# Optimization experiments

Hardware: AMD Instinct MI355X
Metric: run time of the kernel (lower is better)

Reference implementation:

```python
import jax, jax.numpy as jnp
import numpy as np

EPS = 1e-5
NEG = -1e9

def rmsnorm(x, g, eps=EPS):
    x32 = x.astype(jnp.float32)
    n = x32 * jax.lax.rsqrt(jnp.mean(x32 * x32, axis=-1, keepdims=True) + eps)
    return g * n.astype(x.dtype)

def setup_inputs() -> dict:
    key = jax.random.key(0)
    ks = jax.random.split(key, 10)
    B, S, D, H = 2, 2048, 768, 12
    F = 4 * D
    s = 0.02
    return {
        "x": jax.random.normal(ks[0], (B, S, D), jnp.float32),
        "mask": jax.random.randint(ks[1], (B, S, S), 0, 2, jnp.int32),
        "wq": jax.random.normal(ks[2], (D, D), jnp.float32) * s,
        "wk": jax.random.normal(ks[3], (D, D), jnp.float32) * s,
        "wv": jax.random.normal(ks[4], (D, D), jnp.float32) * s,
        "wo": jax.random.normal(ks[5], (D, D), jnp.float32) * s,
        "w1": jax.random.normal(ks[6], (F, D), jnp.float32) * s,
        "w2": jax.random.normal(ks[7], (D, F), jnp.float32) * s,
        "w3": jax.random.normal(ks[8], (F, D), jnp.float32) * s,
        "g_attn": jnp.ones((D,), jnp.float32),
        "g_ffn": jnp.ones((D,), jnp.float32),
    }

def reference(x, mask, wq, wk, wv, wo, w1, w2, w3, g_attn, g_ffn):
    B, S, D = x.shape
    H = 12
    Dk = D // H
    # --- attention sub-block (pre-norm) ---
    xn = rmsnorm(x, g_attn)
    # torch Linear: y = x @ W^T; split heads -> [B,H,S,Dk]
    q = (xn @ wq.T).reshape(B, S, H, Dk).transpose(0, 2, 1, 3)
    k = (xn @ wk.T).reshape(B, S, H, Dk).transpose(0, 2, 1, 3)
    v = (xn @ wv.T).reshape(B, S, H, Dk).transpose(0, 2, 1, 3)
    scores = jnp.einsum("bhqd,bhkd->bhqk", q, k) / jnp.sqrt(jnp.float32(Dk))
    scores = jnp.where(mask[:, None, :, :] == 0, jnp.float32(NEG), scores)
    probs = jax.nn.softmax(scores, axis=-1)  # dropout p=0.0 -> identity
    attn = jnp.einsum("bhqk,bhkd->bhqd", probs, v)
    attn = attn.transpose(0, 2, 1, 3).reshape(B, S, D)
    h = x + attn @ wo.T
    # --- SwiGLU FFN sub-block (pre-norm) ---
    hn = rmsnorm(h, g_ffn)
    ffn = (jax.nn.silu(hn @ w1.T) * (hn @ w3.T)) @ w2.T
    return h + ffn
```

## Files before the change

### kernel.cpp

```cpp
#include <hip/hip_runtime.h>
#include <hip/hip_bf16.h>

#define S_LEN 2048
#define D_MODEL 768
#define NH 12
#define DK 64
#define F_DIM 3072
#define BATCH 2
#define M_ROWS (BATCH * S_LEN)

typedef __bf16 bf16x8 __attribute__((ext_vector_type(8)));
typedef float floatx4 __attribute__((ext_vector_type(4)));
typedef unsigned short u16;
typedef unsigned long long u64;

__device__ inline float bf2f(u16 u) {
    union { unsigned int i; float f; } x; x.i = ((unsigned int)u) << 16; return x.f;
}
__device__ inline u16 f2bf(float f) {
    union { float f; unsigned int i; } x; x.f = f;
    unsigned int r = x.i + 0x7fffu + ((x.i >> 16) & 1u);
    return (u16)(r >> 16);
}
__device__ __forceinline__ bf16x8 as_bf16x8(uint4 v) {
    union { uint4 u; bf16x8 b; } c; c.u = v; return c.b;
}

__device__ __forceinline__ void ldsload16(const u16* g, u16* l) {
    __builtin_amdgcn_global_load_lds(
        (const __attribute__((address_space(1))) unsigned int*)g,
        (__attribute__((address_space(3))) unsigned int*)l, 16, 0, 0);
}

__global__ __launch_bounds__(256)
void cvt_all(const float4* __restrict__ wq, const float4* __restrict__ wk,
             const float4* __restrict__ wv, const float4* __restrict__ wo,
             const float4* __restrict__ w1, const float4* __restrict__ w2,
             const float4* __restrict__ w3,
             ushort4* wqb, ushort4* wkb, ushort4* wvb, ushort4* wob,
             ushort4* w13f, ushort4* w2b) {
    const int WS4 = (D_MODEL * D_MODEL) / 4;
    const int WB4 = (F_DIM * D_MODEL) / 4;
    const int RW4 = D_MODEL / 4;
    int i = blockIdx.x * 256 + threadIdx.x;
    const float4* src; ushort4* dst; int off, doff;
    if (i < 4 * WS4) {
        int s = i / WS4; off = i - s * WS4; doff = off;
        src = (s == 0) ? wq : (s == 1) ? wk : (s == 2) ? wv : wo;
        dst = (s == 0) ? wqb : (s == 1) ? wkb : (s == 2) ? wvb : wob;
    } else {
        int j = i - 4 * WS4; int s = j / WB4; off = j - s * WB4;
        if (s == 1) { src = w2; dst = w2b; doff = off; }
        else {
            src = (s == 0) ? w1 : w3;
            dst = w13f;
            int which = (s == 0) ? 0 : 1;
            int row = off / RW4, c4 = off - row * RW4;
            int k = c4 * 4;
            int n_tile = row >> 4, nl = row & 15;
            int k_tile = k >> 5, quad = (k >> 3) & 3, jj = k & 7;
            int lane = quad * 16 + nl;
            int f = (n_tile * 24 + k_tile) * 2 + which;
            doff = (f * 512 + lane * 8 + jj) >> 2;
        }
    }
    float4 v = src[off];
    ushort4 o;
    o.x = f2bf(v.x); o.y = f2bf(v.y); o.z = f2bf(v.z); o.w = f2bf(v.w);
    dst[doff] = o;
}

__global__ __launch_bounds__(256)
void mask_bits(const int* __restrict__ m, u64* __restrict__ bits) {
    size_t gid = (size_t)blockIdx.x * 256 + threadIdx.x;
    u64 b = __ballot(m[gid] != 0);
    if ((threadIdx.x & 63) == 0) bits[gid >> 6] = b;
}

__global__ __launch_bounds__(256)
void rmsnorm_k(const float* __restrict__ x, const float* __restrict__ g, u16* __restrict__ out) {
    int row = blockIdx.x;
    const float* xr = x + (size_t)row * D_MODEL;
    u16* orow = out + (size_t)row * D_MODEL;
    int t = threadIdx.x;
    float v0 = xr[t];
    float v1 = xr[t + 256];
    float v2 = xr[t + 512];
    float ss = v0 * v0 + v1 * v1 + v2 * v2;
    #pragma unroll
    for (int off = 1; off < 64; off <<= 1) ss += __shfl_xor(ss, off);
    __shared__ float red[4];
    if ((t & 63) == 0) red[t >> 6] = ss;
    __syncthreads();
    float tot = red[0] + red[1] + red[2] + red[3];
    float scale = rsqrtf(tot * (1.0f / (float)D_MODEL) + 1e-5f);
    orow[t]       = f2bf(g[t]       * v0 * scale);
    orow[t + 256] = f2bf(g[t + 256] * v1 * scale);
    orow[t + 512] = f2bf(g[t + 512] * v2 * scale);
}

__global__ __launch_bounds__(256, 3)
void gemm_f1(const u16* __restrict__ A, const u16* __restrict__ W13f,
             u16* __restrict__ Cout) {
    const int K = D_MODEL, N = F_DIM;
    __shared__ u16 As[2][64][32];

    int t = threadIdx.x;
    int w = t >> 6, lane = t & 63;
    int lrow = lane & 15, quad = lane >> 4;

    int lid = blockIdx.y * 24 + blockIdx.x;
    int xcd = lid & 7, s = lid >> 3;
    int nb = xcd * 3 + (s % 3);
    int mb = s / 3;
    int mBase = mb * 64;
    int ntile0 = nb * 8 + w * 2;

    int srow = lane >> 2, scol = (lane & 3) * 8;
    const u16* Ag = A + (size_t)(mBase + w * 16 + srow) * K + scol;
    const uint4* Bf = (const uint4*)W13f;

    auto stageA = [&](int k0, int b) {
        ldsload16(Ag + k0, &As[b][w * 16][0]);
    };

    floatx4 zero = {0.f, 0.f, 0.f, 0.f};
    floatx4 acc[4][2], acc2[4][2];
    #pragma unroll
    for (int r = 0; r < 4; ++r)
        #pragma unroll
        for (int c = 0; c < 2; ++c) { acc[r][c] = zero; acc2[r][c] = zero; }

    stageA(0, 0);
    int cur = 0;
    for (int kt = 0; kt < 24; ++kt) {
        uint4 b1v[2], b3v[2];
        #pragma unroll
        for (int c = 0; c < 2; ++c) {
            int f = ((ntile0 + c) * 24 + kt) * 2;
            b1v[c] = Bf[(size_t)f * 64 + lane];
            b3v[c] = Bf[(size_t)(f + 1) * 64 + lane];
        }
        __syncthreads();
        if (kt + 1 < 24) stageA((kt + 1) * 32, cur ^ 1);

        bf16x8 af[4];
        #pragma unroll
        for (int r = 0; r < 4; ++r) af[r] = *(const bf16x8*)&As[cur][r * 16 + lrow][quad * 8];
        #pragma unroll
        for (int c = 0; c < 2; ++c) {
            bf16x8 b1f = as_bf16x8(b1v[c]);
            bf16x8 b3f = as_bf16x8(b3v[c]);
            #pragma unroll
            for (int r = 0; r < 4; ++r) {
                acc[r][c]  = __builtin_amdgcn_mfma_f32_16x16x32_bf16(af[r], b1f, acc[r][c], 0, 0, 0);
                acc2[r][c] = __builtin_amdgcn_mfma_f32_16x16x32_bf16(af[r], b3f, acc2[r][c], 0, 0, 0);
            }
        }
        cur ^= 1;
    }

    #pragma unroll
    for (int r = 0; r < 4; ++r) {
        #pragma unroll
        for (int c = 0; c < 2; ++c) {
            #pragma unroll
            for (int j = 0; j < 4; ++j) {
                int grow = mBase + r * 16 + quad * 4 + j;
                int gcol = nb * 128 + w * 32 + c * 16 + lrow;
                float a = acc[r][c][j];
                Cout[(size_t)grow * N + gcol] = f2bf((a / (1.0f + __expf(-a))) * acc2[r][c][j]);
            }
        }
    }
}

__global__ __launch_bounds__(256, 3)
void gemm64(const u16* __restrict__ A, const u16* __restrict__ B1,
            const float* __restrict__ R, float* __restrict__ Cout, int N, int K) {
    __shared__ u16 As[2][64][32];
    __shared__ u16 Bs[2][64][32];

    int t = threadIdx.x;
    int w = t >> 6, lane = t & 63;
    int mBase = blockIdx.y * 64, nBase = blockIdx.x * 64;
    int lrow = lane & 15, quad = lane >> 4;
    int wm = (w >> 1) * 32, wn = (w & 1) * 32;

    int srow = lane >> 2, scol = (lane & 3) * 8;
    const u16* Ag = A  + (size_t)(mBase + w * 16 + srow) * K + scol;
    const u16* Bg = B1 + (size_t)(nBase + w * 16 + srow) * K + scol;

    auto stage = [&](int k0, int b) {
        ldsload16(Ag + k0, &As[b][w * 16][0]);
        ldsload16(Bg + k0, &Bs[b][w * 16][0]);
    };

    floatx4 zero = {0.f, 0.f, 0.f, 0.f};
    floatx4 acc[2][2];
    #pragma unroll
    for (int r = 0; r < 2; ++r)
        #pragma unroll
        for (int c = 0; c < 2; ++c) acc[r][c] = zero;

    stage(0, 0);
    int cur = 0;
    for (int k0 = 0; k0 < K; k0 += 32) {
        __syncthreads();
        if (k0 + 32 < K) stage(k0 + 32, cur ^ 1);

        bf16x8 af[2], bf[2];
        #pragma unroll
        for (int r = 0; r < 2; ++r) af[r] = *(const bf16x8*)&As[cur][wm + r * 16 + lrow][quad * 8];
        #pragma unroll
        for (int c = 0; c < 2; ++c) bf[c] = *(const bf16x8*)&Bs[cur][wn + c * 16 + lrow][quad * 8];
        #pragma unroll
        for (int r = 0; r < 2; ++r)
            #pragma unroll
            for (int c = 0; c < 2; ++c)
                acc[r][c] = __builtin_amdgcn_mfma_f32_16x16x32_bf16(af[r], bf[c], acc[r][c], 0, 0, 0);
        cur ^= 1;
    }

    #pragma unroll
    for (int r = 0; r < 2; ++r) {
        #pragma unroll
        for (int c = 0; c < 2; ++c) {
            #pragma unroll
            for (int j = 0; j < 4; ++j) {
                int grow = mBase + wm + r * 16 + quad * 4 + j;
                int gcol = nBase + wn + c * 16 + lrow;
                size_t idx = (size_t)grow * N + gcol;
                Cout[idx] = acc[r][c][j] + R[idx];
            }
        }
    }
}

__global__ __launch_bounds__(256, 4)
void gemm_qkv(const u16* __restrict__ A, const u16* __restrict__ wq,
              const u16* __restrict__ wk, const u16* __restrict__ wv,
              u16* __restrict__ qb, u16* __restrict__ kb, u16* __restrict__ vt) {
    const int K = D_MODEL;
    __shared__ u16 As[2][64][32];
    __shared__ u16 Bs[2][128][32];

    int t = threadIdx.x;
    int w = t >> 6, lane = t & 63;
    int nb = blockIdx.x;
    int which = nb / 6;
    int mBase = blockIdx.y * 64, nBase = (nb % 6) * 128;
    const u16* B1 = (which == 0) ? wq : (which == 1) ? wk : wv;
    int lrow = lane & 15, quad = lane >> 4;
    int wm = (w >> 1) * 32, wn = (w & 1) * 64;

    int srow = lane >> 2, scol = (lane & 3) * 8;
    const u16* Ag = A  + (size_t)(mBase + w * 16 + srow) * K + scol;
    const u16* Bg = B1 + (size_t)(nBase + w * 32 + srow) * K + scol;

    auto stage = [&](int k0, int b) {
        ldsload16(Ag + k0, &As[b][w * 16][0]);
        ldsload16(Bg + k0, &Bs[b][w * 32][0]);
        ldsload16(Bg + (size_t)16 * K + k0, &Bs[b][w * 32 + 16][0]);
    };

    floatx4 zero = {0.f, 0.f, 0.f, 0.f};
    floatx4 acc[2][4];
    #pragma unroll
    for (int r = 0; r < 2; ++r)
        #pragma unroll
        for (int c = 0; c < 4; ++c) acc[r][c] = zero;

    stage(0, 0);
    int cur = 0;
    for (int k0 = 0; k0 < K; k0 += 32) {
        __syncthreads();
        if (k0 + 32 < K) stage(k0 + 32, cur ^ 1);
        bf16x8 af[2];
        #pragma unroll
        for (int r = 0; r < 2; ++r) af[r] = *(const bf16x8*)&As[cur][wm + r * 16 + lrow][quad * 8];
        #pragma unroll
        for (int c = 0; c < 4; ++c) {
            bf16x8 bfr = *(const bf16x8*)&Bs[cur][wn + c * 16 + lrow][quad * 8];
            #pragma unroll
            for (int r = 0; r < 2; ++r)
                acc[r][c] = __builtin_amdgcn_mfma_f32_16x16x32_bf16(af[r], bfr, acc[r][c], 0, 0, 0);
        }
        cur ^= 1;
    }

    u16* dst = (which == 0) ? qb : kb;
    const float qscale = 0.18033688011112042f;
    #pragma unroll
    for (int r = 0; r < 2; ++r) {
        #pragma unroll
        for (int c = 0; c < 4; ++c) {
            #pragma unroll
            for (int j = 0; j < 4; ++j) {
                int grow = mBase + wm + r * 16 + quad * 4 + j;
                int gcol = nBase + wn + c * 16 + lrow;
                float val = acc[r][c][j];
                if (which == 2) {
                    int bb = grow >> 11, s = grow & 2047;
                    int hh = gcol >> 6, d = gcol & 63;
                    vt[((((size_t)bb * NH + hh) * DK + d) << 11) + s] = f2bf(val);
                } else {
                    if (which == 0) val *= qscale;
                    dst[(size_t)grow * D_MODEL + gcol] = f2bf(val);
                }
            }
        }
    }
}

__global__ __launch_bounds__(256)
void attn_mfma(const u16* __restrict__ q, const u16* __restrict__ k,
               const u16* __restrict__ vt, const u64* __restrict__ mbits,
               u16* __restrict__ out) {
    __shared__ u16 Qs0[64][32], Qs1[64][32];
    __shared__ u16 Ks0[64][32], Ks1[64][32];
    __shared__ u16 Vs0[64][32], Vs1[64][32];
    __shared__ u16 PT[4][16][72];

    int t = threadIdx.x;
    int lane = t & 63;
    int w = t >> 6;
    int lrow = lane & 15;
    int quad = lane >> 4;

    int st0 = blockIdx.x * 64;
    int bh = blockIdx.y;
    int h = bh % NH;
    int b = bh / NH;

    const u16* qbase = q + ((size_t)b * S_LEN + st0) * D_MODEL + h * DK;
    const u16* kbase = k + (size_t)b * S_LEN * D_MODEL + h * DK;
    const u16* vbase = vt + (size_t)bh * DK * S_LEN;
    const u64* bw = mbits + ((size_t)b * S_LEN + st0 + w * 16 + lrow) * (S_LEN / 64);

    int srow = lane >> 2;
    int scol = (lane & 3) * 8;

    const u16* qg = qbase + (size_t)(w * 16 + srow) * D_MODEL + scol;
    ldsload16(qg, &Qs0[w * 16][0]);
    ldsload16(qg + 32, &Qs1[w * 16][0]);
    __syncthreads();
    bf16x8 bq0 = *(const bf16x8*)&Qs0[w * 16 + lrow][quad * 8];
    bf16x8 bq1 = *(const bf16x8*)&Qs1[w * 16 + lrow][quad * 8];

    const u16* kg = kbase + (size_t)(w * 16 + srow) * D_MODEL + scol;
    const u16* vg = vbase + (size_t)(w * 16 + srow) * S_LEN + scol;

    bf16x8 ones;
    {
        union { u16 u; __bf16 b; } o; o.u = 0x3F80;
        #pragma unroll
        for (int j = 0; j < 8; ++j) ones[j] = o.b;
    }

    floatx4 zero = {0.f, 0.f, 0.f, 0.f};
    floatx4 Ot[4] = {zero, zero, zero, zero};
    floatx4 Osum = zero;

    for (int kt = 0; kt < S_LEN; kt += 64) {
        u64 mw = bw[kt >> 6];
        unsigned mlo = (unsigned)mw, mhi = (unsigned)(mw >> 32);
        __syncthreads();
        ldsload16(kg + (size_t)kt * D_MODEL, &Ks0[w * 16][0]);
        ldsload16(kg + (size_t)kt * D_MODEL + 32, &Ks1[w * 16][0]);
        ldsload16(vg + kt, &Vs0[w * 16][0]);
        ldsload16(vg + kt + 32, &Vs1[w * 16][0]);
        __syncthreads();

        floatx4 st[4];
        #pragma unroll
        for (int nt = 0; nt < 4; ++nt) {
            bf16x8 ak0 = *(const bf16x8*)&Ks0[nt * 16 + lrow][quad * 8];
            bf16x8 ak1 = *(const bf16x8*)&Ks1[nt * 16 + lrow][quad * 8];
            st[nt] = __builtin_amdgcn_mfma_f32_16x16x32_bf16(ak0, bq0, zero, 0, 0, 0);
            st[nt] = __builtin_amdgcn_mfma_f32_16x16x32_bf16(ak1, bq1, st[nt], 0, 0, 0);
        }

        #pragma unroll
        for (int nt = 0; nt < 4; ++nt) {
            unsigned half = (nt & 2) ? mhi : mlo;
            unsigned tmp = half >> ((nt & 1) * 16 + quad * 4);
            unsigned eu[4];
            #pragma unroll
            for (int j = 0; j < 4; ++j) {
                float e = __builtin_amdgcn_exp2f(st[nt][j]);
                unsigned msk = (unsigned)((int)(tmp << (31 - j)) >> 31);
                eu[j] = __float_as_uint(e) & msk;
            }
            uint2 p;
            p.x = (eu[0] >> 16) | (eu[1] & 0xffff0000u);
            p.y = (eu[2] >> 16) | (eu[3] & 0xffff0000u);
            *(uint2*)&PT[w][lrow][nt * 16 + quad * 4] = p;
        }

        bf16x8 ap0 = *(const bf16x8*)&PT[w][lrow][quad * 8];
        bf16x8 ap1 = *(const bf16x8*)&PT[w][lrow][32 + quad * 8];
        Osum = __builtin_amdgcn_mfma_f32_16x16x32_bf16(ap0, ones, Osum, 0, 0, 0);
        Osum = __builtin_amdgcn_mfma_f32_16x16x32_bf16(ap1, ones, Osum, 0, 0, 0);
        #pragma unroll
        for (int dt = 0; dt < 4; ++dt) {
            bf16x8 bv0 = *(const bf16x8*)&Vs0[dt * 16 + lrow][quad * 8];
            bf16x8 bv1 = *(const bf16x8*)&Vs1[dt * 16 + lrow][quad * 8];
            Ot[dt] = __builtin_amdgcn_mfma_f32_16x16x32_bf16(ap0, bv0, Ot[dt], 0, 0, 0);
            Ot[dt] = __builtin_amdgcn_mfma_f32_16x16x32_bf16(ap1, bv1, Ot[dt], 0, 0, 0);
        }
    }

    float invj[4];
    #pragma unroll
    for (int j = 0; j < 4; ++j) invj[j] = 1.0f / Osum[j];

    u16* obase = out + ((size_t)b * S_LEN + st0 + w * 16) * D_MODEL + h * DK;
    #pragma unroll
    for (int dt = 0; dt < 4; ++dt)
        #pragma unroll
        for (int j = 0; j < 4; ++j)
            obase[(size_t)(quad * 4 + j) * D_MODEL + dt * 16 + lrow] = f2bf(Ot[dt][j] * invj[j]);
}

extern "C" void kernel_launch(void* const* d_in, const int* in_sizes, int n_in,
                              void* d_out, int out_size, void* d_ws, size_t ws_size,
                              hipStream_t stream) {
    const float* x      = (const float*)d_in[0];
    const int*   mask   = (const int*)d_in[1];
    const float* wq     = (const float*)d_in[2];
    const float* wk     = (const float*)d_in[3];
    const float* wv     = (const float*)d_in[4];
    const float* wo     = (const float*)d_in[5];
    const float* w1     = (const float*)d_in[6];
    const float* w2     = (const float*)d_in[7];
    const float* w3     = (const float*)d_in[8];
    const float* g_attn = (const float*)d_in[9];
    const float* g_ffn  = (const float*)d_in[10];
    float* out = (float*)d_out;

    const size_t WSMALL = (size_t)D_MODEL * D_MODEL;
    const size_t WBIG   = (size_t)F_DIM * D_MODEL;
    const size_t MD     = (size_t)M_ROWS * D_MODEL;

    char* ws = (char*)d_ws;
    u16* wqb  = (u16*)ws;            ws += WSMALL * 2;
    u16* wkb  = (u16*)ws;            ws += WSMALL * 2;
    u16* wvb  = (u16*)ws;            ws += WSMALL * 2;
    u16* wob  = (u16*)ws;            ws += WSMALL * 2;
    u16* w13f = (u16*)ws;            ws += WBIG * 2 * 2;
    u16* w2b  = (u16*)ws;            ws += WBIG * 2;
    u16* xn  = (u16*)ws;             ws += MD * 2;
    u16* qb  = (u16*)ws;             ws += MD * 2;
    u16* kb  = (u16*)ws;             ws += MD * 2;
    u16* vb  = (u16*)ws;             ws += MD * 2;
    u16* ao  = (u16*)ws;             ws += MD * 2;
    float* hb = (float*)ws;          ws += MD * 4;
    u64* mb  = (u64*)ws;             ws += (size_t)BATCH * S_LEN * (S_LEN / 64) * 8;
    u16* hn = xn;
    u16* ub = qb;
    (void)ws_size; (void)n_in; (void)in_sizes; (void)out_size;

    dim3 blk(256);

    cvt_all<<<9216, blk, 0, stream>>>((const float4*)wq, (const float4*)wk, (const float4*)wv,
                                      (const float4*)wo, (const float4*)w1, (const float4*)w2,
                                      (const float4*)w3,
                                      (ushort4*)wqb, (ushort4*)wkb, (ushort4*)wvb, (ushort4*)wob,
                                      (ushort4*)w13f, (ushort4*)w2b);
    mask_bits<<<(BATCH * S_LEN * S_LEN) / 256, blk, 0, stream>>>(mask, mb);

    rmsnorm_k<<<M_ROWS, blk, 0, stream>>>(x, g_attn, xn);
    gemm_qkv<<<dim3(18, M_ROWS / 64), blk, 0, stream>>>(xn, wqb, wkb, wvb, qb, kb, vb);
    attn_mfma<<<dim3(S_LEN / 64, BATCH * NH), blk, 0, stream>>>(qb, kb, vb, mb, ao);
    gemm64<<<dim3(D_MODEL / 64, M_ROWS / 64), blk, 0, stream>>>(ao, wob, x, hb, D_MODEL, D_MODEL);
    rmsnorm_k<<<M_ROWS, blk, 0, stream>>>((const float*)hb, g_ffn, hn);
    gemm_f1<<<dim3(24, M_ROWS / 64), blk, 0, stream>>>(hn, w13f, ub);
    gemm64<<<dim3(D_MODEL / 64, M_ROWS / 64), blk, 0, stream>>>(ub, w2b, hb, out, D_MODEL, F_DIM);
}
```

Measured before the change: 360.1 us.

## Pre-swizzle all weights into MFMA fragment layout and load B directly from global

Result: no change. 366.0 us (+1.6%).

```diff
diff --git a/kernel.cpp b/kernel.cpp
--- a/kernel.cpp
+++ b/kernel.cpp
@@ -37,31 +37,35 @@
              const float4* __restrict__ wv, const float4* __restrict__ wo,
              const float4* __restrict__ w1, const float4* __restrict__ w2,
              const float4* __restrict__ w3,
-             ushort4* wqb, ushort4* wkb, ushort4* wvb, ushort4* wob,
-             ushort4* w13f, ushort4* w2b) {
+             ushort4* wqf, ushort4* wkf, ushort4* wvf, ushort4* wof,
+             ushort4* w13f, ushort4* w2f) {
     const int WS4 = (D_MODEL * D_MODEL) / 4;
     const int WB4 = (F_DIM * D_MODEL) / 4;
-    const int RW4 = D_MODEL / 4;
     int i = blockIdx.x * 256 + threadIdx.x;
     const float4* src; ushort4* dst; int off, doff;
     if (i < 4 * WS4) {
-        int s = i / WS4; off = i - s * WS4; doff = off;
+        int s = i / WS4; off = i - s * WS4;
         src = (s == 0) ? wq : (s == 1) ? wk : (s == 2) ? wv : wo;
-        dst = (s == 0) ? wqb : (s == 1) ? wkb : (s == 2) ? wvb : wob;
+        dst = (s == 0) ? wqf : (s == 1) ? wkf : (s == 2) ? wvf : wof;
+        int row = off / 192, c4 = off - row * 192;
+        int k = c4 * 4;
+        int lane = ((k >> 3) & 3) * 16 + (row & 15);
+        doff = (((row >> 4) * 24 + (k >> 5)) * 512 + lane * 8 + (k & 7)) >> 2;
     } else {
         int j = i - 4 * WS4; int s = j / WB4; off = j - s * WB4;
-        if (s == 1) { src = w2; dst = w2b; doff = off; }
-        else {
-            src = (s == 0) ? w1 : w3;
-            dst = w13f;
+        if (s == 1) {
+            src = w2; dst = w2f;
+            int row = off / 768, c4 = off - row * 768;
+            int k = c4 * 4;
+            int lane = ((k >> 3) & 3) * 16 + (row & 15);
+            doff = (((row >> 4) * 96 + (k >> 5)) * 512 + lane * 8 + (k & 7)) >> 2;
+        } else {
             int which = (s == 0) ? 0 : 1;
-            int row = off / RW4, c4 = off - row * RW4;
+            src = (s == 0) ? w1 : w3; dst = w13f;
+            int row = off / 192, c4 = off - row * 192;
             int k = c4 * 4;
-            int n_tile = row >> 4, nl = row & 15;
-            int k_tile = k >> 5, quad = (k >> 3) & 3, jj = k & 7;
-            int lane = quad * 16 + nl;
-            int f = (n_tile * 24 + k_tile) * 2 + which;
-            doff = (f * 512 + lane * 8 + jj) >> 2;
+            int lane = ((k >> 3) & 3) * 16 + (row & 15);
+            doff = ((((row >> 4) * 24 + (k >> 5)) * 2 + which) * 512 + lane * 8 + (k & 7)) >> 2;
         }
     }
     float4 v = src[off];
@@ -103,7 +107,7 @@
 void gemm_f1(const u16* __restrict__ A, const u16* __restrict__ W13f,
              u16* __restrict__ Cout) {
     const int K = D_MODEL, N = F_DIM;
-    __shared__ u16 As[2][64][32];
+    __shared__ u16 As[2][4][512];
 
     int t = threadIdx.x;
     int w = t >> 6, lane = t & 63;
@@ -112,17 +116,12 @@
     int lid = blockIdx.y * 24 + blockIdx.x;
     int xcd = lid & 7, s = lid >> 3;
     int nb = xcd * 3 + (s % 3);
-    int mb = s / 3;
-    int mBase = mb * 64;
+    int mBase = (s / 3) * 64;
     int ntile0 = nb * 8 + w * 2;
 
-    int srow = lane >> 2, scol = (lane & 3) * 8;
-    const u16* Ag = A + (size_t)(mBase + w * 16 + srow) * K + scol;
+    const u16* Ag = A + (size_t)(mBase + w * 16 + lrow) * K + quad * 8;
     const uint4* Bf = (const uint4*)W13f;
-
-    auto stageA = [&](int k0, int b) {
-        ldsload16(Ag + k0, &As[b][w * 16][0]);
-    };
+    auto stageA = [&](int k0, int b) { ldsload16(Ag + k0, &As[b][w][0]); };
 
     floatx4 zero = {0.f, 0.f, 0.f, 0.f};
     floatx4 acc[4][2], acc2[4][2];
@@ -146,7 +145,7 @@
 
         bf16x8 af[4];
         #pragma unroll
-        for (int r = 0; r < 4; ++r) af[r] = *(const bf16x8*)&As[cur][r * 16 + lrow][quad * 8];
+        for (int r = 0; r < 4; ++r) af[r] = *(const bf16x8*)&As[cur][r][lane * 8];
         #pragma unroll
         for (int c = 0; c < 2; ++c) {
             bf16x8 b1f = as_bf16x8(b1v[c]);
@@ -175,26 +174,22 @@
     }
 }
 
-__global__ __launch_bounds__(256, 3)
-void gemm64(const u16* __restrict__ A, const u16* __restrict__ B1,
-            const float* __restrict__ R, float* __restrict__ Cout, int N, int K) {
-    __shared__ u16 As[2][64][32];
-    __shared__ u16 Bs[2][64][32];
+__global__ __launch_bounds__(256, 4)
+void gemm_nf(const u16* __restrict__ A, const u16* __restrict__ Bw,
+             const float* __restrict__ R, float* __restrict__ Cout, int N, int K) {
+    const int KT = K >> 5;
+    __shared__ u16 As[2][4][512];
 
     int t = threadIdx.x;
     int w = t >> 6, lane = t & 63;
+    int lrow = lane & 15, quad = lane >> 4;
     int mBase = blockIdx.y * 64, nBase = blockIdx.x * 64;
-    int lrow = lane & 15, quad = lane >> 4;
-    int wm = (w >> 1) * 32, wn = (w & 1) * 32;
-
-    int srow = lane >> 2, scol = (lane & 3) * 8;
-    const u16* Ag = A  + (size_t)(mBase + w * 16 + srow) * K + scol;
-    const u16* Bg = B1 + (size_t)(nBase + w * 16 + srow) * K + scol;
-
-    auto stage = [&](int k0, int b) {
-        ldsload16(Ag + k0, &As[b][w * 16][0]);
-        ldsload16(Bg + k0, &Bs[b][w * 16][0]);
-    };
+    int wm = (w >> 1) * 2, wn = (w & 1) * 2;
+    int ntile0 = (nBase >> 4) + wn;
+
+    const u16* Ag = A + (size_t)(mBase + w * 16 + lrow) * K + quad * 8;
+    const uint4* Bf = (const uint4*)Bw;
+    auto stageA = [&](int k0, int b) { ldsload16(Ag + k0, &As[b][w][0]); };
 
     floatx4 zero = {0.f, 0.f, 0.f, 0.f};
     floatx4 acc[2][2];
@@ -203,22 +198,26 @@
         #pragma unroll
         for (int c = 0; c < 2; ++c) acc[r][c] = zero;
 
-    stage(0, 0);
+    stageA(0, 0);
     int cur = 0;
-    for (int k0 = 0; k0 < K; k0 += 32) {
+    for (int kt = 0; kt < KT; ++kt) {
+        uint4 bv[2];
+        #pragma unroll
+        for (int c = 0; c < 2; ++c)
+            bv[c] = Bf[(size_t)((ntile0 + c) * KT + kt) * 64 + lane];
         __syncthreads();
-        if (k0 + 32 < K) stage(k0 + 32, cur ^ 1);
-
-        bf16x8 af[2], bf[2];
-        #pragma unroll
-        for (int r = 0; r < 2; ++r) af[r] = *(const bf16x8*)&As[cur][wm + r * 16 + lrow][quad * 8];
-        #pragma unroll
-        for (int c = 0; c < 2; ++c) bf[c] = *(const bf16x8*)&Bs[cur][wn + c * 16 + lrow][quad * 8];
-        #pragma unroll
-        for (int r = 0; r < 2; ++r)
-            #pragma unroll
-            for (int c = 0; c < 2; ++c)
-                acc[r][c] = __builtin_amdgcn_mfma_f32_16x16x32_bf16(af[r], bf[c], acc[r][c], 0, 0, 0);
+        if (kt + 1 < KT) stageA((kt + 1) * 32, cur ^ 1);
+
+        bf16x8 af[2];
+        #pragma unroll
+        for (int r = 0; r < 2; ++r) af[r] = *(const bf16x8*)&As[cur][wm + r][lane * 8];
+        #pragma unroll
+        for (int c = 0; c < 2; ++c) {
+            bf16x8 bfr = as_bf16x8(bv[c]);
+            #pragma unroll
+            for (int r = 0; r < 2; ++r)
+                acc[r][c] = __builtin_amdgcn_mfma_f32_16x16x32_bf16(af[r], bfr, acc[r][c], 0, 0, 0);
+        }
         cur ^= 1;
     }
 
@@ -228,8 +227,8 @@
         for (int c = 0; c < 2; ++c) {
             #pragma unroll
             for (int j = 0; j < 4; ++j) {
-                int grow = mBase + wm + r * 16 + quad * 4 + j;
-                int gcol = nBase + wn + c * 16 + lrow;
+                int grow = mBase + (wm + r) * 16 + quad * 4 + j;
+                int gcol = nBase + (wn + c) * 16 + lrow;
                 size_t idx = (size_t)grow * N + gcol;
                 Cout[idx] = acc[r][c][j] + R[idx];
             }
@@ -238,52 +237,48 @@
 }
 
 __global__ __launch_bounds__(256, 4)
-void gemm_qkv(const u16* __restrict__ A, const u16* __restrict__ wq,
-              const u16* __restrict__ wk, const u16* __restrict__ wv,
+void gemm_qkv(const u16* __restrict__ A, const u16* __restrict__ wqf,
+              const u16* __restrict__ wkf, const u16* __restrict__ wvf,
               u16* __restrict__ qb, u16* __restrict__ kb, u16* __restrict__ vt) {
-    const int K = D_MODEL;
-    __shared__ u16 As[2][64][32];
-    __shared__ u16 Bs[2][128][32];
+    const int K = D_MODEL, KT = 24;
+    __shared__ u16 As[2][4][512];
 
     int t = threadIdx.x;
     int w = t >> 6, lane = t & 63;
-    int nb = blockIdx.x;
-    int which = nb / 6;
-    int mBase = blockIdx.y * 64, nBase = (nb % 6) * 128;
-    const u16* B1 = (which == 0) ? wq : (which == 1) ? wk : wv;
     int lrow = lane & 15, quad = lane >> 4;
-    int wm = (w >> 1) * 32, wn = (w & 1) * 64;
-
-    int srow = lane >> 2, scol = (lane & 3) * 8;
-    const u16* Ag = A  + (size_t)(mBase + w * 16 + srow) * K + scol;
-    const u16* Bg = B1 + (size_t)(nBase + w * 32 + srow) * K + scol;
-
-    auto stage = [&](int k0, int b) {
-        ldsload16(Ag + k0, &As[b][w * 16][0]);
-        ldsload16(Bg + k0, &Bs[b][w * 32][0]);
-        ldsload16(Bg + (size_t)16 * K + k0, &Bs[b][w * 32 + 16][0]);
-    };
+    int nb = blockIdx.x, which = nb / 6, nbl = nb % 6;
+    int mBase = blockIdx.y * 64;
+    const uint4* Bf = (const uint4*)((which == 0) ? wqf : (which == 1) ? wkf : wvf);
+    int ntile0 = nbl * 8 + w * 2;
+
+    const u16* Ag = A + (size_t)(mBase + w * 16 + lrow) * K + quad * 8;
+    auto stageA = [&](int k0, int b) { ldsload16(Ag + k0, &As[b][w][0]); };
 
     floatx4 zero = {0.f, 0.f, 0.f, 0.f};
-    floatx4 acc[2][4];
-    #pragma unroll
-    for (int r = 0; r < 2; ++r)
-        #pragma unroll
-        for (int c = 0; c < 4; ++c) acc[r][c] = zero;
-
-    stage(0, 0);
+    floatx4 acc[4][2];
+    #pragma unroll
+    for (int r = 0; r < 4; ++r)
+        #pragma unroll
+        for (int c = 0; c < 2; ++c) acc[r][c] = zero;
+
+    stageA(0, 0);
     int cur = 0;
-    for (int k0 = 0; k0 < K; k0 += 32) {
+    for (int kt = 0; kt < KT; ++kt) {
+        uint4 bv[2];
+        #pragma unroll
+        for (int c = 0; c < 2; ++c)
+            bv[c] = Bf[(size_t)((ntile0 + c) * KT + kt) * 64 + lane];
         __syncthreads();
-        if (k0 + 32 < K) stage(k0 + 32, cur ^ 1);
-        bf16x8 af[2];
-        #pragma unroll
-        for (int r = 0; r < 2; ++r) af[r] = *(const bf16x8*)&As[cur][wm + r * 16 + lrow][quad * 8];
-        #pragma unroll
-        for (int c = 0; c < 4; ++c) {
-            bf16x8 bfr = *(const bf16x8*)&Bs[cur][wn + c * 16 + lrow][quad * 8];
-            #pragma unroll
-            for (int r = 0; r < 2; ++r)
+        if (kt + 1 < KT) stageA((kt + 1) * 32, cur ^ 1);
+
+        bf16x8 af[4];
+        #pragma unroll
+        for (int r = 0; r < 4; ++r) af[r] = *(const bf16x8*)&As[cur][r][lane * 8];
+        #pragma unroll
+        for (int c = 0; c < 2; ++c) {
+            bf16x8 bfr = as_bf16x8(bv[c]);
+            #pragma unroll
+            for (int r = 0; r < 4; ++r)
                 acc[r][c] = __builtin_amdgcn_mfma_f32_16x16x32_bf16(af[r], bfr, acc[r][c], 0, 0, 0);
         }
         cur ^= 1;
@@ -292,13 +287,13 @@
     u16* dst = (which == 0) ? qb : kb;
     const float qscale = 0.18033688011112042f;
     #pragma unroll
-    for (int r = 0; r < 2; ++r) {
-        #pragma unroll
-        for (int c = 0; c < 4; ++c) {
+    for (int r = 0; r < 4; ++r) {
+        #pragma unroll
+        for (int c = 0; c < 2; ++c) {
             #pragma unroll
             for (int j = 0; j < 4; ++j) {
-                int grow = mBase + wm + r * 16 + quad * 4 + j;
-                int gcol = nBase + wn + c * 16 + lrow;
+                int grow = mBase + r * 16 + quad * 4 + j;
+                int gcol = nbl * 128 + w * 32 + c * 16 + lrow;
                 float val = acc[r][c][j];
                 if (which == 2) {
                     int bb = grow >> 11, s = grow & 2047;
@@ -317,9 +312,9 @@
 void attn_mfma(const u16* __restrict__ q, const u16* __restrict__ k,
                const u16* __restrict__ vt, const u64* __restrict__ mbits,
                u16* __restrict__ out) {
-    __shared__ u16 Qs0[64][32], Qs1[64][32];
-    __shared__ u16 Ks0[64][32], Ks1[64][32];
-    __shared__ u16 Vs0[64][32], Vs1[64][32];
+    __shared__ u16 Qs0[4][512], Qs1[4][512];
+    __shared__ u16 Ks0[4][512], Ks1[4][512];
+    __shared__ u16 Vs0[4][512], Vs1[4][512];
     __shared__ u16 PT[4][16][72];
 
     int t = threadIdx.x;
@@ -333,23 +328,16 @@
     int h = bh % NH;
     int b = bh / NH;
 
-    const u16* qbase = q + ((size_t)b * S_LEN + st0) * D_MODEL + h * DK;
-    const u16* kbase = k + (size_t)b * S_LEN * D_MODEL + h * DK;
-    const u16* vbase = vt + (size_t)bh * DK * S_LEN;
+    const u16* qg = q + ((size_t)(b * S_LEN + st0 + w * 16 + lrow)) * D_MODEL + h * DK + quad * 8;
+    const u16* kg = k + ((size_t)(b * S_LEN + w * 16 + lrow)) * D_MODEL + h * DK + quad * 8;
+    const u16* vg = vt + (size_t)bh * DK * S_LEN + (size_t)(w * 16 + lrow) * S_LEN + quad * 8;
     const u64* bw = mbits + ((size_t)b * S_LEN + st0 + w * 16 + lrow) * (S_LEN / 64);
 
-    int srow = lane >> 2;
-    int scol = (lane & 3) * 8;
-
-    const u16* qg = qbase + (size_t)(w * 16 + srow) * D_MODEL + scol;
-    ldsload16(qg, &Qs0[w * 16][0]);
-    ldsload16(qg + 32, &Qs1[w * 16][0]);
+    ldsload16(qg, &Qs0[w][0]);
+    ldsload16(qg + 32, &Qs1[w][0]);
     __syncthreads();
-    bf16x8 bq0 = *(const bf16x8*)&Qs0[w * 16 + lrow][quad * 8];
-    bf16x8 bq1 = *(const bf16x8*)&Qs1[w * 16 + lrow][quad * 8];
-
-    const u16* kg = kbase + (size_t)(w * 16 + srow) * D_MODEL + scol;
-    const u16* vg = vbase + (size_t)(w * 16 + srow) * S_LEN + scol;
+    bf16x8 bq0 = *(const bf16x8*)&Qs0[w][lane * 8];
+    bf16x8 bq1 = *(const bf16x8*)&Qs1[w][lane * 8];
 
     bf16x8 ones;
     {
@@ -366,17 +354,17 @@
         u64 mw = bw[kt >> 6];
         unsigned mlo = (unsigned)mw, mhi = (unsigned)(mw >> 32);
         __syncthreads();
-        ldsload16(kg + (size_t)kt * D_MODEL, &Ks0[w * 16][0]);
-        ldsload16(kg + (size_t)kt * D_MODEL + 32, &Ks1[w * 16][0]);
-        ldsload16(vg + kt, &Vs0[w * 16][0]);
-        ldsload16(vg + kt + 32, &Vs1[w * 16][0]);
+        ldsload16(kg + (size_t)kt * D_MODEL, &Ks0[w][0]);
+        ldsload16(kg + (size_t)kt * D_MODEL + 32, &Ks1[w][0]);
+        ldsload16(vg + kt, &Vs0[w][0]);
+        ldsload16(vg + kt + 32, &Vs1[w][0]);
         __syncthreads();
 
         floatx4 st[4];
         #pragma unroll
         for (int nt = 0; nt < 4; ++nt) {
-            bf16x8 ak0 = *(const bf16x8*)&Ks0[nt * 16 + lrow][quad * 8];
-            bf16x8 ak1 = *(const bf16x8*)&Ks1[nt * 16 + lrow][quad * 8];
+            bf16x8 ak0 = *(const bf16x8*)&Ks0[nt][lane * 8];
+            bf16x8 ak1 = *(const bf16x8*)&Ks1[nt][lane * 8];
             st[nt] = __builtin_amdgcn_mfma_f32_16x16x32_bf16(ak0, bq0, zero, 0, 0, 0);
             st[nt] = __builtin_amdgcn_mfma_f32_16x16x32_bf16(ak1, bq1, st[nt], 0, 0, 0);
         }
@@ -404,8 +392,8 @@
         Osum = __builtin_amdgcn_mfma_f32_16x16x32_bf16(ap1, ones, Osum, 0, 0, 0);
         #pragma unroll
         for (int dt = 0; dt < 4; ++dt) {
-            bf16x8 bv0 = *(const bf16x8*)&Vs0[dt * 16 + lrow][quad * 8];
-            bf16x8 bv1 = *(const bf16x8*)&Vs1[dt * 16 + lrow][quad * 8];
+            bf16x8 bv0 = *(const bf16x8*)&Vs0[dt][lane * 8];
+            bf16x8 bv1 = *(const bf16x8*)&Vs1[dt][lane * 8];
             Ot[dt] = __builtin_amdgcn_mfma_f32_16x16x32_bf16(ap0, bv0, Ot[dt], 0, 0, 0);
             Ot[dt] = __builtin_amdgcn_mfma_f32_16x16x32_bf16(ap1, bv1, Ot[dt], 0, 0, 0);
         }
@@ -444,12 +432,12 @@
     const size_t MD     = (size_t)M_ROWS * D_MODEL;
 
     char* ws = (char*)d_ws;
-    u16* wqb  = (u16*)ws;            ws += WSMALL * 2;
-    u16* wkb  = (u16*)ws;            ws += WSMALL * 2;
-    u16* wvb  = (u16*)ws;            ws += WSMALL * 2;
-    u16* wob  = (u16*)ws;            ws += WSMALL * 2;
+    u16* wqf  = (u16*)ws;            ws += WSMALL * 2;
+    u16* wkf  = (u16*)ws;            ws += WSMALL * 2;
+    u16* wvf  = (u16*)ws;            ws += WSMALL * 2;
+    u16* wof  = (u16*)ws;            ws += WSMALL * 2;
     u16* w13f = (u16*)ws;            ws += WBIG * 2 * 2;
-    u16* w2b  = (u16*)ws;            ws += WBIG * 2;
+    u16* w2f  = (u16*)ws;            ws += WBIG * 2;
     u16* xn  = (u16*)ws;             ws += MD * 2;
     u16* qb  = (u16*)ws;             ws += MD * 2;
     u16* kb  = (u16*)ws;             ws += MD * 2;
@@ -466,15 +454,15 @@
     cvt_all<<<9216, blk, 0, stream>>>((const float4*)wq, (const float4*)wk, (const float4*)wv,
                                       (const float4*)wo, (const float4*)w1, (const float4*)w2,
                                       (const float4*)w3,
-                                      (ushort4*)wqb, (ushort4*)wkb, (ushort4*)wvb, (ushort4*)wob,
-                                      (ushort4*)w13f, (ushort4*)w2b);
+                                      (ushort4*)wqf, (ushort4*)wkf, (ushort4*)wvf, (ushort4*)wof,
+                                      (ushort4*)w13f, (ushort4*)w2f);
     mask_bits<<<(BATCH * S_LEN * S_LEN) / 256, blk, 0, stream>>>(mask, mb);
 
     rmsnorm_k<<<M_ROWS, blk, 0, stream>>>(x, g_attn, xn);
-    gemm_qkv<<<dim3(18, M_ROWS / 64), blk, 0, stream>>>(xn, wqb, wkb, wvb, qb, kb, vb);
+    gemm_qkv<<<dim3(18, M_ROWS / 64), blk, 0, stream>>>(xn, wqf, wkf, wvf, qb, kb, vb);
     attn_mfma<<<dim3(S_LEN / 64, BATCH * NH), blk, 0, stream>>>(qb, kb, vb, mb, ao);
-    gemm64<<<dim3(D_MODEL / 64, M_ROWS / 64), blk, 0, stream>>>(ao, wob, x, hb, D_MODEL, D_MODEL);
+    gemm_nf<<<dim3(D_MODEL / 64, M_ROWS / 64), blk, 0, stream>>>(ao, wof, x, hb, D_MODEL, D_MODEL);
     rmsnorm_k<<<M_ROWS, blk, 0, stream>>>((const float*)hb, g_ffn, hn);
     gemm_f1<<<dim3(24, M_ROWS / 64), blk, 0, stream>>>(hn, w13f, ub);
-    gemm64<<<dim3(D_MODEL / 64, M_ROWS / 64), blk, 0, stream>>>(ub, w2b, hb, out, D_MODEL, F_DIM);
-}
+    gemm_nf<<<dim3(D_MODEL / 64, M_ROWS / 64), blk, 0, stream>>>(ub, w2f, hb, out, D_MODEL, F_DIM);
+}
```
